# Kernel optimization log

Measured on AMD Instinct MI355X. Metric: run time of the kernel, lower is better.

Reference implementation:

```python
import jax, jax.numpy as jnp
import numpy as np

N, E, D, H, OUT, L, G = 50000, 800000, 128, 128, 128, 5, 512
EMB = L * H  # 640
BN_EPS = 1e-5


def setup_inputs() -> dict:
    key = jax.random.key(0)
    ks = jax.random.split(key, 24)
    s_h = 1.0 / np.sqrt(H)
    s_e = 1.0 / np.sqrt(EMB)
    inp = {
        'x': jax.random.normal(ks[0], (N, D), jnp.float32),
        'edge_index': jax.random.randint(ks[1], (2, E), 0, N, jnp.int32),
        'batch': jnp.sort(jax.random.randint(ks[2], (N,), 0, G, jnp.int32)),
        # per-layer GINConv MLP: Linear(D/H->H), BN(H), ReLU, Linear(H->H). D==H so stackable.
        'conv_W1': jax.random.normal(ks[3], (L, H, H), jnp.float32) * s_h,
        'conv_b1': jnp.zeros((L, H), jnp.float32),
        'conv_g1': jnp.ones((L, H), jnp.float32),
        'conv_be1': jnp.zeros((L, H), jnp.float32),
        'conv_W2': jax.random.normal(ks[4], (L, H, H), jnp.float32) * s_h,
        'conv_b2': jnp.zeros((L, H), jnp.float32),
        'eps': jnp.zeros((L,), jnp.float32),  # train_eps=True, init 0.0
        # outer BatchNorm per layer
        'bn_g': jnp.ones((L, H), jnp.float32),
        'bn_b': jnp.zeros((L, H), jnp.float32),
        # per-layer prediction heads Linear(H -> OUT)
        'pred_W': jax.random.normal(ks[5], (L, H, OUT), jnp.float32) * s_h,
        'pred_b': jnp.zeros((L, OUT), jnp.float32),
        # global_d FF(EMB): 3 stacked Linear(EMB,EMB) + shortcut
        'gW': jax.random.normal(ks[6], (3, EMB, EMB), jnp.float32) * s_e,
        'gb': jnp.zeros((3, EMB), jnp.float32),
        'gsW': jax.random.normal(ks[7], (EMB, EMB), jnp.float32) * s_e,
        'gsb': jnp.zeros((EMB,), jnp.float32),
        # local_d FF(EMB)
        'lW': jax.random.normal(ks[8], (3, EMB, EMB), jnp.float32) * s_e,
        'lb': jnp.zeros((3, EMB), jnp.float32),
        'lsW': jax.random.normal(ks[9], (EMB, EMB), jnp.float32) * s_e,
        'lsb': jnp.zeros((EMB,), jnp.float32),
    }
    return inp


def _bn(h, g, b):
    # BatchNorm1d, training mode: batch stats over node dim (biased var)
    m = jnp.mean(h, axis=0)
    v = jnp.var(h, axis=0)
    return g * (h - m) * jax.lax.rsqrt(v + BN_EPS) + b


def _ff(x, W, b, Ws, bs):
    h = x
    for i in range(3):
        h = jax.nn.relu(h @ W[i] + b[i])
    return h + x @ Ws + bs


def reference(x, edge_index, batch, conv_W1, conv_b1, conv_g1, conv_be1,
              conv_W2, conv_b2, eps, bn_g, bn_b, pred_W, pred_b,
              gW, gb, gsW, gsb, lW, lb, lsW, lsb):
    src, dst = edge_index[0], edge_index[1]
    h = x
    xs = []
    for i in range(L):
        # GINConv: (1+eps)*x_i + sum_{j->i} x_j, then MLP
        agg = jax.ops.segment_sum(h[src], dst, num_segments=N)
        h = (1.0 + eps[i]) * h + agg
        h = _bn(h @ conv_W1[i] + conv_b1[i], conv_g1[i], conv_be1[i])
        h = jax.nn.relu(h)
        h = h @ conv_W2[i] + conv_b2[i]
        h = jax.nn.relu(_bn(h, bn_g[i], bn_b[i]))
        xs.append(h)
    # per-layer graph sum-pool + prediction head (dropout in eval = identity)
    xpool = [jax.ops.segment_sum(xs[i], batch, num_segments=G) @ pred_W[i] + pred_b[i]
             for i in range(L)]
    xcat = jnp.concatenate(xpool, axis=1)            # [G, L*OUT]
    graph_embedding = _ff(xcat, gW, gb, gsW, gsb)     # [G, EMB]
    node_embedding = _ff(jnp.concatenate(xs, axis=1), lW, lb, lsW, lsb)  # [N, EMB]
    return (graph_embedding, node_embedding, xcat)
```

## Files before the change

kernel.cpp:

```cpp
#include <hip/hip_runtime.h>

constexpr int H    = 128;
constexpr int LNUM = 5;
constexpr int NG   = 512;
constexpr int EMB  = 640;
constexpr float BN_EPS = 1e-5f;

typedef __attribute__((ext_vector_type(8))) short bf16x8;
typedef __attribute__((ext_vector_type(4))) float f32x4;

__device__ inline unsigned short f2bf(float f){
  unsigned u = __builtin_bit_cast(unsigned, f);
  u += 0x7FFF + ((u >> 16) & 1);
  return (unsigned short)(u >> 16);
}
__device__ inline float bf2f(unsigned short h){
  unsigned u = ((unsigned)h) << 16;
  return __builtin_bit_cast(float, u);
}

__device__ inline int xcd_swz(int bid, int nwg){
  int q = nwg >> 3, r = nwg & 7;
  int xcd = bid & 7, idx = bid >> 3;
  return (xcd < r ? xcd*(q+1) : r*(q+1) + (xcd-r)*q) + idx;
}

__global__ void k_zerof(float* p, int n){
  int i = blockIdx.x*256 + threadIdx.x;
  if (i < n) p[i] = 0.f;
}
__global__ void k_zeroi(int* p, int n){
  int i = blockIdx.x*256 + threadIdx.x;
  if (i < n) p[i] = 0;
}

__global__ void k_hist(const int* __restrict__ dst, int E, int* deg){
  int e = blockIdx.x*256 + threadIdx.x;
  if (e < E) atomicAdd(&deg[dst[e]], 1);
}

__global__ __launch_bounds__(1024) void k_scan(int* degcur, int* __restrict__ rowptr, int n){
  __shared__ int wsum[16];
  __shared__ int carry;
  int tid = threadIdx.x, wid = tid >> 6, lane = tid & 63;
  if (tid == 0){ carry = 0; rowptr[0] = 0; }
  __syncthreads();
  for (int base = 0; base < n; base += 1024){
    int v = (base + tid < n) ? degcur[base + tid] : 0;
    int s = v;
#pragma unroll
    for (int off = 1; off < 64; off <<= 1){
      int t = __shfl_up(s, off);
      if (lane >= off) s += t;
    }
    if (lane == 63) wsum[wid] = s;
    __syncthreads();
    if (wid == 0 && lane < 16){
      int wv = wsum[lane];
#pragma unroll
      for (int off = 1; off < 16; off <<= 1){
        int t = __shfl_up(wv, off);
        if (lane >= off) wv += t;
      }
      wsum[lane] = wv;
    }
    __syncthreads();
    int incl = s + (wid ? wsum[wid-1] : 0) + carry;
    if (base + tid < n){ rowptr[base + tid + 1] = incl; degcur[base + tid] = incl - v; }
    __syncthreads();
    if (tid == 0) carry += wsum[15];
    __syncthreads();
  }
}

__global__ void k_scatter(const int* __restrict__ src, const int* __restrict__ dst,
                          int E, int* cursor, int* __restrict__ colsrc){
  int e = blockIdx.x*256 + threadIdx.x;
  if (e < E){
    int d = dst[e];
    int pos = atomicAdd(&cursor[d], 1);
    colsrc[pos] = src[e];
  }
}

__global__ void k_gstart(const int* __restrict__ batch, int N, int* __restrict__ gstart){
  int g = blockIdx.x*256 + threadIdx.x;
  if (g <= NG){
    int lo = 0, hi = N;
    while (lo < hi){
      int mid = (lo + hi) >> 1;
      if (batch[mid] < g) lo = mid + 1; else hi = mid;
    }
    gstart[g] = lo;
  }
}

__global__ void k_castT(const float* __restrict__ W, unsigned short* __restrict__ Wt,
                        int K, int Nn, int ldt, int koff){
  __shared__ float sh[32][33];
  const size_t in_off  = (size_t)blockIdx.z * K * Nn;
  const size_t out_off = (size_t)blockIdx.z * Nn * ldt;
  int n0 = blockIdx.x*32, k0 = blockIdx.y*32;
  int tx = threadIdx.x, ty = threadIdx.y;
  for (int r = ty; r < 32; r += 8)
    sh[r][tx] = W[in_off + (size_t)(k0 + r)*Nn + n0 + tx];
  __syncthreads();
  for (int r = ty; r < 32; r += 8)
    Wt[out_off + (size_t)(n0 + r)*ldt + koff + k0 + tx] = f2bf(sh[tx][r]);
}

__global__ void k_bias2(const float* __restrict__ a, const float* __restrict__ b,
                        float* __restrict__ o){
  int i = threadIdx.x;
  o[i] = a[i] + b[i];
}

template<bool IN_BF16>
__global__ __launch_bounds__(256) void k_agg(const void* __restrict__ hin_, int ldh,
                                             const int* __restrict__ rowptr,
                                             const int* __restrict__ colsrc,
                                             const float* __restrict__ epsp,
                                             unsigned short* __restrict__ outp, int nN){
  int node = blockIdx.x*4 + (threadIdx.x >> 6);
  if (node >= nN) return;
  int lane = threadIdx.x & 63;
  float a0, a1;
  if (IN_BF16){
    unsigned u = ((const unsigned*)hin_)[((size_t)node*ldh >> 1) + lane];
    a0 = bf2f((unsigned short)u); a1 = bf2f((unsigned short)(u >> 16));
  } else {
    float2 f = ((const float2*)hin_)[((size_t)node*ldh >> 1) + lane];
    a0 = f.x; a1 = f.y;
  }
  float ep = 1.0f + *epsp;
  a0 *= ep; a1 *= ep;
  int e = rowptr[node], e1 = rowptr[node+1];
  const int ld2 = ldh >> 1;
  for (; e + 4 <= e1; e += 4){
    int s0 = colsrc[e], s1 = colsrc[e+1], s2 = colsrc[e+2], s3 = colsrc[e+3];
    if (IN_BF16){
      unsigned u0 = ((const unsigned*)hin_)[(size_t)s0*ld2 + lane];
      unsigned u1 = ((const unsigned*)hin_)[(size_t)s1*ld2 + lane];
      unsigned u2 = ((const unsigned*)hin_)[(size_t)s2*ld2 + lane];
      unsigned u3 = ((const unsigned*)hin_)[(size_t)s3*ld2 + lane];
      a0 += bf2f((unsigned short)u0) + bf2f((unsigned short)u1)
          + bf2f((unsigned short)u2) + bf2f((unsigned short)u3);
      a1 += bf2f((unsigned short)(u0 >> 16)) + bf2f((unsigned short)(u1 >> 16))
          + bf2f((unsigned short)(u2 >> 16)) + bf2f((unsigned short)(u3 >> 16));
    } else {
      float2 f0 = ((const float2*)hin_)[(size_t)s0*ld2 + lane];
      float2 f1 = ((const float2*)hin_)[(size_t)s1*ld2 + lane];
      float2 f2 = ((const float2*)hin_)[(size_t)s2*ld2 + lane];
      float2 f3 = ((const float2*)hin_)[(size_t)s3*ld2 + lane];
      a0 += f0.x + f1.x + f2.x + f3.x;
      a1 += f0.y + f1.y + f2.y + f3.y;
    }
  }
  for (; e < e1; ++e){
    int s = colsrc[e];
    if (IN_BF16){
      unsigned u = ((const unsigned*)hin_)[(size_t)s*ld2 + lane];
      a0 += bf2f((unsigned short)u); a1 += bf2f((unsigned short)(u >> 16));
    } else {
      float2 f = ((const float2*)hin_)[(size_t)s*ld2 + lane];
      a0 += f.x; a1 += f.y;
    }
  }
  ((unsigned*)outp)[((size_t)node*H >> 1) + lane] =
      (unsigned)f2bf(a0) | ((unsigned)f2bf(a1) << 16);
}

__global__ void k_bnfin(float* sums, float* sumsq,
                        const float* __restrict__ g, const float* __restrict__ b,
                        float* __restrict__ scale, float* __restrict__ shift, float invn){
  int c = threadIdx.x;
  float m = sums[c]*invn;
  float v = sumsq[c]*invn - m*m;
  float inv = rsqrtf(v + BN_EPS);
  float sc = g[c]*inv;
  scale[c] = sc;
  shift[c] = b[c] - m*sc;
  sums[c] = 0.f; sumsq[c] = 0.f;
}

__global__ __launch_bounds__(256) void k_bnapply(const unsigned short* __restrict__ U,
                                                 const float* __restrict__ scale,
                                                 const float* __restrict__ shift,
                                                 unsigned short* __restrict__ out,
                                                 int ldo, int n){
  int i = blockIdx.x*256 + threadIdx.x;
  int total = n * (H/4);
  if (i < total){
    int r = i >> 5;
    int c4 = (i & 31) << 2;
    uint2 up = *(const uint2*)(U + (size_t)r*H + c4);
    float4 sc = *(const float4*)(scale + c4);
    float4 sf = *(const float4*)(shift + c4);
    float a = fmaxf(fmaf(sc.x, bf2f((unsigned short)up.x),        sf.x), 0.f);
    float b = fmaxf(fmaf(sc.y, bf2f((unsigned short)(up.x>>16)),  sf.y), 0.f);
    float c = fmaxf(fmaf(sc.z, bf2f((unsigned short)up.y),        sf.z), 0.f);
    float d = fmaxf(fmaf(sc.w, bf2f((unsigned short)(up.y>>16)),  sf.w), 0.f);
    uint2 o;
    o.x = (unsigned)f2bf(a) | ((unsigned)f2bf(b) << 16);
    o.y = (unsigned)f2bf(c) | ((unsigned)f2bf(d) << 16);
    *(uint2*)(out + (size_t)r*ldo + c4) = o;
  }
}

__global__ __launch_bounds__(320) void k_pool(const unsigned short* __restrict__ xall,
                                              const int* __restrict__ gstart,
                                              float* __restrict__ pooled){
  int g = blockIdx.x;
  int t = threadIdx.x;
  int n0 = gstart[g], n1 = gstart[g+1];
  float a0 = 0.f, a1 = 0.f;
  for (int n = n0; n < n1; ++n){
    unsigned u = ((const unsigned*)xall)[(size_t)n*(EMB/2) + t];
    a0 += bf2f((unsigned short)u); a1 += bf2f((unsigned short)(u >> 16));
  }
  *(float2*)(pooled + (size_t)g*EMB + 2*t) = make_float2(a0, a1);
}

__global__ __launch_bounds__(128) void k_pred(const float* __restrict__ pooled,
                                              const float* __restrict__ W,
                                              const float* __restrict__ b,
                                              float* __restrict__ xcat){
  int g = blockIdx.x, l = blockIdx.y, o = threadIdx.x;
  __shared__ float sh[128];
  sh[o] = pooled[(size_t)g*EMB + l*H + o];
  __syncthreads();
  const float* Wl = W + (size_t)l*H*H;
  float acc = b[l*H + o];
  for (int k = 0; k < H; ++k) acc = fmaf(sh[k], Wl[k*H + o], acc);
  xcat[(size_t)g*EMB + l*H + o] = acc;
}

template<bool RELU, bool OUT_BF16, bool DUAL>
__global__ __launch_bounds__(512) void k_mm(
    const unsigned short* __restrict__ A, int lda,
    const unsigned short* __restrict__ A2,
    const unsigned short* __restrict__ Bt, int ldb,
    const float* __restrict__ bias,
    void* __restrict__ Cv, int ldc,
    int M, int K)
{
  __shared__ union LdsU {
    unsigned short stage[2][2][128*64];
    unsigned short sc16[128*136];
    float          sc32[128*132];
  } u;
  const int tid  = threadIdx.x;
  const int lane = tid & 63;
  const int w    = tid >> 6;
  const int wr   = w >> 2, wc = w & 3;

  const int nwg = gridDim.x * gridDim.y;
  const int bid = blockIdx.y * gridDim.x + blockIdx.x;
  const int wg  = xcd_swz(bid, nwg);
  const int col0 = (wg % gridDim.x) * 128;
  const int row0 = (wg / gridDim.x) * 128;
  const int KA   = DUAL ? (K >> 1) : K;

  const unsigned short *sA[2], *sA2[2], *sB[2];
  int dOff[2];
#pragma unroll
  for (int j = 0; j < 2; ++j){
    int d = w*2048 + j*1024 + lane*16;
    int m = d >> 7;
    int inner = (d & 127) ^ ((m & 7) << 4);
    int gm = row0 + m; if (gm > M-1) gm = M-1;
    sA[j]  = A  + (size_t)gm*lda + (inner >> 1);
    if (DUAL) sA2[j] = A2 + (size_t)gm*lda + (inner >> 1);
    sB[j]  = Bt + (size_t)(col0 + m)*ldb + (inner >> 1);
    dOff[j] = w*2048 + j*1024;
  }

  f32x4 acc[4][2];
#pragma unroll
  for (int i = 0; i < 4; ++i)
#pragma unroll
    for (int j = 0; j < 2; ++j)
      acc[i][j] = (f32x4){0.f, 0.f, 0.f, 0.f};

  auto STAGE = [&](int buf, int kt){
    int k0 = kt*64;
    int ka = k0;
    bool second = DUAL && (k0 >= KA);
    if (second) ka = k0 - KA;
#pragma unroll
    for (int j = 0; j < 2; ++j){
      const unsigned short* srcA = second ? (sA2[j] + ka) : (sA[j] + ka);
      __builtin_amdgcn_global_load_lds(
          (const __attribute__((address_space(1))) void*)srcA,
          (__attribute__((address_space(3))) void*)((char*)&u.stage[buf][0][0] + dOff[j]),
          16, 0, 0);
    }
#pragma unroll
    for (int j = 0; j < 2; ++j)
      __builtin_amdgcn_global_load_lds(
          (const __attribute__((address_space(1))) void*)(sB[j] + k0),
          (__attribute__((address_space(3))) void*)((char*)&u.stage[buf][1][0] + dOff[j]),
          16, 0, 0);
  };

  auto COMPUTE = [&](int buf){
    const char* Ab = (const char*)&u.stage[buf][0][0];
    const char* Bb = (const char*)&u.stage[buf][1][0];
#pragma unroll
    for (int kk = 0; kk < 2; ++kk){
      const int kb = kk*64 + ((lane >> 4) << 4);
      bf16x8 af[4], bfr[2];
#pragma unroll
      for (int i = 0; i < 4; ++i){
        int row = wr*64 + i*16 + (lane & 15);
        int ab  = (row*128 + kb) ^ ((row & 7) << 4);
        af[i] = *(const bf16x8*)(Ab + ab);
      }
#pragma unroll
      for (int j = 0; j < 2; ++j){
        int col = wc*32 + j*16 + (lane & 15);
        int bb  = (col*128 + kb) ^ ((col & 7) << 4);
        bfr[j] = *(const bf16x8*)(Bb + bb);
      }
#pragma unroll
      for (int i = 0; i < 4; ++i)
#pragma unroll
        for (int j = 0; j < 2; ++j)
          acc[i][j] = __builtin_amdgcn_mfma_f32_16x16x32_bf16(af[i], bfr[j], acc[i][j], 0, 0, 0);
    }
  };

  const int NT = K / 64;
  STAGE(0, 0);
  STAGE(1, 1);
  asm volatile("s_waitcnt vmcnt(4)" ::: "memory");
  __syncthreads();

  int cur = 0;
  for (int t = 0; t < NT; ++t){
    COMPUTE(cur);
    if (t == NT-1) break;
    __syncthreads();
    if (t + 2 < NT){
      STAGE(cur, t + 2);
      asm volatile("s_waitcnt vmcnt(4)" ::: "memory");
    } else {
      asm volatile("s_waitcnt vmcnt(0)" ::: "memory");
    }
    __syncthreads();
    cur ^= 1;
  }

  __syncthreads();
  if (OUT_BF16){
#pragma unroll
    for (int j = 0; j < 2; ++j){
      int cl = wc*32 + j*16 + (lane & 15);
      float bs = bias[col0 + cl];
#pragma unroll
      for (int i = 0; i < 4; ++i){
        int rb = wr*64 + i*16 + ((lane >> 4) << 2);
#pragma unroll
        for (int r = 0; r < 4; ++r){
          float v = acc[i][j][r] + bs;
          if (RELU) v = fmaxf(v, 0.f);
          u.sc16[(rb + r)*136 + cl] = f2bf(v);
        }
      }
    }
    __syncthreads();
    unsigned short* Cb = (unsigned short*)Cv;
    for (int idx = tid; idx < 128*16; idx += 512){
      int rr = idx >> 4, seg = idx & 15;
      int grow = row0 + rr;
      if (grow < M){
        uint4 vv = *(const uint4*)&u.sc16[rr*136 + seg*8];
        *(uint4*)(Cb + (size_t)grow*ldc + col0 + seg*8) = vv;
      }
    }
  } else {
#pragma unroll
    for (int j = 0; j < 2; ++j){
      int cl = wc*32 + j*16 + (lane & 15);
      float bs = bias[col0 + cl];
#pragma unroll
      for (int i = 0; i < 4; ++i){
        int rb = wr*64 + i*16 + ((lane >> 4) << 2);
#pragma unroll
        for (int r = 0; r < 4; ++r){
          float v = acc[i][j][r] + bs;
          if (RELU) v = fmaxf(v, 0.f);
          u.sc32[(rb + r)*132 + cl] = v;
        }
      }
    }
    __syncthreads();
    float* Cf = (float*)Cv;
    for (int idx = tid; idx < 128*32; idx += 512){
      int rr = idx >> 5, seg = idx & 31;
      int grow = row0 + rr;
      if (grow < M){
        float4 vv = *(const float4*)&u.sc32[rr*132 + seg*4];
        *(float4*)(Cf + (size_t)grow*ldc + col0 + seg*4) = vv;
      }
    }
  }
}

template<bool PRO_BN, bool STATS>
__global__ __launch_bounds__(512) void k_mmc(
    const unsigned short* __restrict__ A,
    const unsigned short* __restrict__ Bt,
    const float* __restrict__ bias,
    const float* __restrict__ kscale, const float* __restrict__ kshift,
    unsigned short* __restrict__ C, int ldc,
    float* sums, float* sumsq,
    int M)
{
  __shared__ unsigned short shm[2*128*128];
  unsigned short* As = shm;
  unsigned short* Bs = shm + 128*128;
  const int tid  = threadIdx.x;
  const int lane = tid & 63;
  const int w    = tid >> 6;
  const int wr   = w >> 2, wc = w & 3;

  const int wg   = xcd_swz(blockIdx.x, gridDim.x);
  const int row0 = wg * 128;

#pragma unroll
  for (int j = 0; j < 4; ++j){
    int d = w*4096 + j*1024 + lane*16;
    int m = d >> 8;
    int inner = (d & 255) ^ ((m & 15) << 4);
    int gm = row0 + m; if (gm > M-1) gm = M-1;
    __builtin_amdgcn_global_load_lds(
        (const __attribute__((address_space(1))) void*)(A + (size_t)gm*H + (inner >> 1)),
        (__attribute__((address_space(3))) void*)((char*)As + w*4096 + j*1024),
        16, 0, 0);
    __builtin_amdgcn_global_load_lds(
        (const __attribute__((address_space(1))) void*)(Bt + (size_t)m*H + (inner >> 1)),
        (__attribute__((address_space(3))) void*)((char*)Bs + w*4096 + j*1024),
        16, 0, 0);
  }
  asm volatile("s_waitcnt vmcnt(0)" ::: "memory");
  __syncthreads();

  f32x4 acc[4][2];
#pragma unroll
  for (int i = 0; i < 4; ++i)
#pragma unroll
    for (int j = 0; j < 2; ++j)
      acc[i][j] = (f32x4){0.f, 0.f, 0.f, 0.f};

#pragma unroll
  for (int kk = 0; kk < 4; ++kk){
    const int kb = kk*64 + ((lane >> 4) << 4);
    bf16x8 af[4], bfr[2];
#pragma unroll
    for (int i = 0; i < 4; ++i){
      int row = wr*64 + i*16 + (lane & 15);
      int ab  = (row*256 + kb) ^ ((row & 15) << 4);
      af[i] = *(const bf16x8*)((const char*)As + ab);
    }
#pragma unroll
    for (int j = 0; j < 2; ++j){
      int col = wc*32 + j*16 + (lane & 15);
      int bb  = (col*256 + kb) ^ ((col & 15) << 4);
      bfr[j] = *(const bf16x8*)((const char*)Bs + bb);
    }
    if (PRO_BN){
      int k8 = kk*32 + ((lane >> 4) << 3);
      float4 s0 = *(const float4*)(kscale + k8), s1 = *(const float4*)(kscale + k8 + 4);
      float4 f0 = *(const float4*)(kshift + k8), f1 = *(const float4*)(kshift + k8 + 4);
      float sc[8] = {s0.x,s0.y,s0.z,s0.w,s1.x,s1.y,s1.z,s1.w};
      float sf[8] = {f0.x,f0.y,f0.z,f0.w,f1.x,f1.y,f1.z,f1.w};
#pragma unroll
      for (int i = 0; i < 4; ++i){
        bf16x8 a = af[i], o;
#pragma unroll
        for (int jj = 0; jj < 8; ++jj){
          float v = fmaxf(fmaf(sc[jj], bf2f((unsigned short)a[jj]), sf[jj]), 0.f);
          o[jj] = (short)f2bf(v);
        }
        af[i] = o;
      }
    }
#pragma unroll
    for (int i = 0; i < 4; ++i)
#pragma unroll
      for (int j = 0; j < 2; ++j)
        acc[i][j] = __builtin_amdgcn_mfma_f32_16x16x32_bf16(af[i], bfr[j], acc[i][j], 0, 0, 0);
  }

  if (STATS){
#pragma unroll
    for (int j = 0; j < 2; ++j){
      int col = wc*32 + j*16 + (lane & 15);
      float bs = bias[col];
      float s = 0.f, q = 0.f;
#pragma unroll
      for (int i = 0; i < 4; ++i){
        int rb = row0 + wr*64 + i*16 + ((lane >> 4) << 2);
#pragma unroll
        for (int r = 0; r < 4; ++r){
          if (rb + r < M){
            float v = acc[i][j][r] + bs;
            s += v; q += v*v;
          }
        }
      }
      s += __shfl_xor(s, 16); q += __shfl_xor(q, 16);
      s += __shfl_xor(s, 32); q += __shfl_xor(q, 32);
      if (lane < 16){
        atomicAdd(&sums[col], s);
        atomicAdd(&sumsq[col], q);
      }
    }
  }

  __syncthreads();
#pragma unroll
  for (int j = 0; j < 2; ++j){
    int cl = wc*32 + j*16 + (lane & 15);
    float bs = bias[cl];
#pragma unroll
    for (int i = 0; i < 4; ++i){
      int rb = wr*64 + i*16 + ((lane >> 4) << 2);
#pragma unroll
      for (int r = 0; r < 4; ++r)
        shm[(rb + r)*136 + cl] = f2bf(acc[i][j][r] + bs);
    }
  }
  __syncthreads();
  for (int idx = tid; idx < 128*16; idx += 512){
    int rr = idx >> 4, seg = idx & 15;
    int grow = row0 + rr;
    if (grow < M){
      uint4 vv = *(const uint4*)&shm[rr*136 + seg*8];
      *(uint4*)(C + (size_t)grow*ldc + seg*8) = vv;
    }
  }
}

template<bool RELU, bool ADD_D>
__global__ __launch_bounds__(256) void k_gemm64(
    const float* __restrict__ A, int lda,
    const float* __restrict__ B, int ldb,
    const float* __restrict__ bias,
    const float* D, int ldd,
    float* C, int ldc,
    int M, int N, int K)
{
  __shared__ float As[32][68];
  __shared__ float Bs[32][64];
  const int tid  = threadIdx.x;
  const int tx   = tid & 15;
  const int ty   = tid >> 4;
  const int row0 = blockIdx.x * 64;
  const int col0 = blockIdx.y * 64;
  const int am = tid >> 3;
  const int ak = (tid & 7) << 2;
  const int bk = tid >> 4;
  const int bn = (tid & 15) << 2;
  float acc[4][4] = {};

  for (int k0 = 0; k0 < K; k0 += 32){
#pragma unroll
    for (int h = 0; h < 2; ++h){
      int m  = am + h*32;
      int gr = row0 + m;
      float4 v = make_float4(0.f, 0.f, 0.f, 0.f);
      if (gr < M) v = *(const float4*)(A + (size_t)gr*lda + k0 + ak);
      As[ak+0][m]=v.x; As[ak+1][m]=v.y; As[ak+2][m]=v.z; As[ak+3][m]=v.w;
    }
#pragma unroll
    for (int h = 0; h < 2; ++h){
      int kk = bk + h*16;
      *(float4*)(&Bs[kk][bn]) = *(const float4*)(B + (size_t)(k0+kk)*ldb + col0 + bn);
    }
    __syncthreads();
#pragma unroll 8
    for (int k = 0; k < 32; ++k){
      float4 a = *(const float4*)(&As[k][ty<<2]);
      float4 b = *(const float4*)(&Bs[k][tx<<2]);
      float av[4] = {a.x,a.y,a.z,a.w};
      float bv[4] = {b.x,b.y,b.z,b.w};
#pragma unroll
      for (int i = 0; i < 4; ++i)
#pragma unroll
        for (int j = 0; j < 4; ++j)
          acc[i][j] = fmaf(av[i], bv[j], acc[i][j]);
    }
    __syncthreads();
  }

  const int col = col0 + (tx<<2);
  float4 bv = *(const float4*)(bias + col);
#pragma unroll
  for (int i = 0; i < 4; ++i){
    int row = row0 + (ty<<2) + i;
    if (row < M){
      float r[4] = {acc[i][0]+bv.x, acc[i][1]+bv.y, acc[i][2]+bv.z, acc[i][3]+bv.w};
      if (RELU){
#pragma unroll
        for (int j = 0; j < 4; ++j) r[j] = fmaxf(r[j], 0.f);
      }
      if (ADD_D){
        float4 d = *(const float4*)(D + (size_t)row*ldd + col);
        r[0]+=d.x; r[1]+=d.y; r[2]+=d.z; r[3]+=d.w;
      }
      *(float4*)(C + (size_t)row*ldc + col) = make_float4(r[0],r[1],r[2],r[3]);
    }
  }
}

extern "C" void kernel_launch(void* const* d_in, const int* in_sizes, int n_in,
                              void* d_out, int out_size, void* d_ws, size_t ws_size,
                              hipStream_t stream) {
  const float* x        = (const float*)d_in[0];
  const int*   ei       = (const int*)d_in[1];
  const int*   batch    = (const int*)d_in[2];
  const float* conv_W1  = (const float*)d_in[3];
  const float* conv_b1  = (const float*)d_in[4];
  const float* conv_g1  = (const float*)d_in[5];
  const float* conv_be1 = (const float*)d_in[6];
  const float* conv_W2  = (const float*)d_in[7];
  const float* conv_b2  = (const float*)d_in[8];
  const float* epsv     = (const float*)d_in[9];
  const float* bn_g     = (const float*)d_in[10];
  const float* bn_b     = (const float*)d_in[11];
  const float* pred_W   = (const float*)d_in[12];
  const float* pred_b   = (const float*)d_in[13];
  const float* gW       = (const float*)d_in[14];
  const float* gb       = (const float*)d_in[15];
  const float* gsW      = (const float*)d_in[16];
  const float* gsb      = (const float*)d_in[17];
  const float* lW       = (const float*)d_in[18];
  const float* lb       = (const float*)d_in[19];
  const float* lsW      = (const float*)d_in[20];
  const float* lsb      = (const float*)d_in[21];

  const int N = in_sizes[0] / H;
  const int E = in_sizes[1] / 2;
  const int* srcI = ei;
  const int* dstI = ei + E;

  float* out = (float*)d_out;
  float* GE = out;
  float* NE = out + (size_t)NG*EMB;
  float* XC = NE + (size_t)N*EMB;

  unsigned short* xall = (unsigned short*)d_ws;
  unsigned short* h1   = xall + (size_t)N*EMB;
  unsigned short* h2   = h1 + (size_t)N*EMB;
  unsigned short* hpre = h1;
  unsigned short* ub   = h1 + (size_t)N*H;
  unsigned short* tb   = h1 + (size_t)2*N*H;

  float* pooled  = (float*)(h2 + (size_t)N*EMB);
  float* gtmp1   = pooled + (size_t)NG*EMB;
  float* gtmp2   = gtmp1 + (size_t)NG*EMB;
  float* sums    = gtmp2 + (size_t)NG*EMB;
  float* sumsq   = sums + 128;
  float* bnscale = sumsq + 128;
  float* bnshift = bnscale + 128;
  float* biasNE  = bnshift + 128;
  unsigned short* W1t   = (unsigned short*)(biasNE + EMB);
  unsigned short* W2t   = W1t + (size_t)LNUM*H*H;
  unsigned short* lWt01 = W2t + (size_t)LNUM*H*H;
  unsigned short* Wcat  = lWt01 + (size_t)2*EMB*EMB;
  int* rowptr = (int*)(Wcat + (size_t)2*EMB*EMB);
  int* cursor = rowptr + (N + 1);
  int* colsrc = cursor + N;
  int* gstart = colsrc + E;

  k_zerof<<<1, 256, 0, stream>>>(sums, 256);

  k_zeroi<<<(N+255)/256, 256, 0, stream>>>(cursor, N);
  k_hist<<<(E+255)/256, 256, 0, stream>>>(dstI, E, cursor);
  k_scan<<<1, 1024, 0, stream>>>(cursor, rowptr, N);
  k_scatter<<<(E+255)/256, 256, 0, stream>>>(srcI, dstI, E, cursor, colsrc);
  k_gstart<<<(NG+256)/256, 256, 0, stream>>>(batch, N, gstart);

  const dim3 tb32(32, 8);
  k_castT<<<dim3(H/32, H/32, LNUM), tb32, 0, stream>>>(conv_W1, W1t, H, H, H, 0);
  k_castT<<<dim3(H/32, H/32, LNUM), tb32, 0, stream>>>(conv_W2, W2t, H, H, H, 0);
  k_castT<<<dim3(EMB/32, EMB/32, 2), tb32, 0, stream>>>(lW, lWt01, EMB, EMB, EMB, 0);
  k_castT<<<dim3(EMB/32, EMB/32, 1), tb32, 0, stream>>>(lW + (size_t)2*EMB*EMB, Wcat,
                                                        EMB, EMB, 2*EMB, 0);
  k_castT<<<dim3(EMB/32, EMB/32, 1), tb32, 0, stream>>>(lsW, Wcat, EMB, EMB, 2*EMB, EMB);
  k_bias2<<<1, EMB, 0, stream>>>(lb + (size_t)2*EMB, lsb, biasNE);

  const float invn = 1.0f / (float)N;
  const int nrow = (N + 127)/128;

  for (int l = 0; l < LNUM; ++l){
    if (l == 0)
      k_agg<false><<<(N+3)/4, 256, 0, stream>>>(x, H, rowptr, colsrc, epsv, hpre, N);
    else
      k_agg<true><<<(N+3)/4, 256, 0, stream>>>(xall + (size_t)(l-1)*H, EMB, rowptr, colsrc,
                                               epsv + l, hpre, N);

    k_mmc<false,true><<<nrow, 512, 0, stream>>>(
        hpre, W1t + (size_t)l*H*H, conv_b1 + l*H, nullptr, nullptr,
        ub, H, sums, sumsq, N);
    k_bnfin<<<1, 128, 0, stream>>>(sums, sumsq, conv_g1 + l*H, conv_be1 + l*H,
                                   bnscale, bnshift, invn);
    k_mmc<true,true><<<nrow, 512, 0, stream>>>(
        ub, W2t + (size_t)l*H*H, conv_b2 + l*H, bnscale, bnshift,
        tb, H, sums, sumsq, N);
    k_bnfin<<<1, 128, 0, stream>>>(sums, sumsq, bn_g + l*H, bn_b + l*H,
                                   bnscale, bnshift, invn);
    k_bnapply<<<(N*32 + 255)/256, 256, 0, stream>>>(tb, bnscale, bnshift,
                                                    xall + (size_t)l*H, EMB, N);
  }

  k_pool<<<NG, 320, 0, stream>>>(xall, gstart, pooled);
  k_pred<<<dim3(NG, LNUM), 128, 0, stream>>>(pooled, pred_W, pred_b, XC);

  const dim3 gg((NG + 63)/64, EMB/64);
  k_gemm64<false,false><<<gg, 256, 0, stream>>>(XC, EMB, gsW, EMB, gsb,
                                                nullptr, 0, GE, EMB, NG, EMB, EMB);
  k_gemm64<true,false><<<gg, 256, 0, stream>>>(XC, EMB, gW, EMB, gb,
                                               nullptr, 0, gtmp1, EMB, NG, EMB, EMB);
  k_gemm64<true,false><<<gg, 256, 0, stream>>>(gtmp1, EMB, gW + (size_t)EMB*EMB, EMB, gb + EMB,
                                               nullptr, 0, gtmp2, EMB, NG, EMB, EMB);
  k_gemm64<true,true><<<gg, 256, 0, stream>>>(gtmp2, EMB, gW + (size_t)2*EMB*EMB, EMB, gb + 2*EMB,
                                              GE, EMB, GE, EMB, NG, EMB, EMB);

  const dim3 gn(EMB/128, nrow);
  k_mm<true,true,false><<<gn, 512, 0, stream>>>(
      xall, EMB, nullptr, lWt01, EMB, lb, h1, EMB, N, EMB);
  k_mm<true,true,false><<<gn, 512, 0, stream>>>(
      h1, EMB, nullptr, lWt01 + (size_t)EMB*EMB, EMB, lb + EMB, h2, EMB, N, EMB);
  k_mm<false,false,true><<<gn, 512, 0, stream>>>(
      h2, EMB, xall, Wcat, 2*EMB, biasNE, NE, EMB, N, 2*EMB);
}
```

Before: 1.181 ms.

## Fuse neighbor aggregation into first GIN matmul and fold BN finalize into consumers

Neighbor aggregation now runs inside the first per-layer matmul kernel. Each thread gathers 32 features of one node, sums over its neighbors, and writes the bf16 result straight into the LDS A tile, so the hpre buffer is never written to or read back from global memory. BN finalize kernels are removed: the scale and shift are computed from per-layer stat slots inside the second matmul and inside bnapply. Separately, the large node-FF GEMM switches to 32-wide K tiles with a 4-deep LDS ring and a different swizzle. The fused gather uses one thread per 32 columns with a serial neighbor loop, which may expose gather latency and lower occupancy compared with the old wavefront-per-node kernel.

```diff
diff --git a/kernel.cpp b/kernel.cpp
--- a/kernel.cpp
+++ b/kernel.cpp
@@ -113,98 +113,6 @@
                         float* __restrict__ o){
   int i = threadIdx.x;
   o[i] = a[i] + b[i];
-}
-
-template<bool IN_BF16>
-__global__ __launch_bounds__(256) void k_agg(const void* __restrict__ hin_, int ldh,
-                                             const int* __restrict__ rowptr,
-                                             const int* __restrict__ colsrc,
-                                             const float* __restrict__ epsp,
-                                             unsigned short* __restrict__ outp, int nN){
-  int node = blockIdx.x*4 + (threadIdx.x >> 6);
-  if (node >= nN) return;
-  int lane = threadIdx.x & 63;
-  float a0, a1;
-  if (IN_BF16){
-    unsigned u = ((const unsigned*)hin_)[((size_t)node*ldh >> 1) + lane];
-    a0 = bf2f((unsigned short)u); a1 = bf2f((unsigned short)(u >> 16));
-  } else {
-    float2 f = ((const float2*)hin_)[((size_t)node*ldh >> 1) + lane];
-    a0 = f.x; a1 = f.y;
-  }
-  float ep = 1.0f + *epsp;
-  a0 *= ep; a1 *= ep;
-  int e = rowptr[node], e1 = rowptr[node+1];
-  const int ld2 = ldh >> 1;
-  for (; e + 4 <= e1; e += 4){
-    int s0 = colsrc[e], s1 = colsrc[e+1], s2 = colsrc[e+2], s3 = colsrc[e+3];
-    if (IN_BF16){
-      unsigned u0 = ((const unsigned*)hin_)[(size_t)s0*ld2 + lane];
-      unsigned u1 = ((const unsigned*)hin_)[(size_t)s1*ld2 + lane];
-      unsigned u2 = ((const unsigned*)hin_)[(size_t)s2*ld2 + lane];
-      unsigned u3 = ((const unsigned*)hin_)[(size_t)s3*ld2 + lane];
-      a0 += bf2f((unsigned short)u0) + bf2f((unsigned short)u1)
-          + bf2f((unsigned short)u2) + bf2f((unsigned short)u3);
-      a1 += bf2f((unsigned short)(u0 >> 16)) + bf2f((unsigned short)(u1 >> 16))
-          + bf2f((unsigned short)(u2 >> 16)) + bf2f((unsigned short)(u3 >> 16));
-    } else {
-      float2 f0 = ((const float2*)hin_)[(size_t)s0*ld2 + lane];
-      float2 f1 = ((const float2*)hin_)[(size_t)s1*ld2 + lane];
-      float2 f2 = ((const float2*)hin_)[(size_t)s2*ld2 + lane];
-      float2 f3 = ((const float2*)hin_)[(size_t)s3*ld2 + lane];
-      a0 += f0.x + f1.x + f2.x + f3.x;
-      a1 += f0.y + f1.y + f2.y + f3.y;
-    }
-  }
-  for (; e < e1; ++e){
-    int s = colsrc[e];
-    if (IN_BF16){
-      unsigned u = ((const unsigned*)hin_)[(size_t)s*ld2 + lane];
-      a0 += bf2f((unsigned short)u); a1 += bf2f((unsigned short)(u >> 16));
-    } else {
-      float2 f = ((const float2*)hin_)[(size_t)s*ld2 + lane];
-      a0 += f.x; a1 += f.y;
-    }
-  }
-  ((unsigned*)outp)[((size_t)node*H >> 1) + lane] =
-      (unsigned)f2bf(a0) | ((unsigned)f2bf(a1) << 16);
-}
-
-__global__ void k_bnfin(float* sums, float* sumsq,
-                        const float* __restrict__ g, const float* __restrict__ b,
-                        float* __restrict__ scale, float* __restrict__ shift, float invn){
-  int c = threadIdx.x;
-  float m = sums[c]*invn;
-  float v = sumsq[c]*invn - m*m;
-  float inv = rsqrtf(v + BN_EPS);
-  float sc = g[c]*inv;
-  scale[c] = sc;
-  shift[c] = b[c] - m*sc;
-  sums[c] = 0.f; sumsq[c] = 0.f;
-}
-
-__global__ __launch_bounds__(256) void k_bnapply(const unsigned short* __restrict__ U,
-                                                 const float* __restrict__ scale,
-                                                 const float* __restrict__ shift,
-                                                 unsigned short* __restrict__ out,
-                                                 int ldo, int n){
-  int i = blockIdx.x*256 + threadIdx.x;
-  int total = n * (H/4);
-  if (i < total){
-    int r = i >> 5;
-    int c4 = (i & 31) << 2;
-    uint2 up = *(const uint2*)(U + (size_t)r*H + c4);
-    float4 sc = *(const float4*)(scale + c4);
-    float4 sf = *(const float4*)(shift + c4);
-    float a = fmaxf(fmaf(sc.x, bf2f((unsigned short)up.x),        sf.x), 0.f);
-    float b = fmaxf(fmaf(sc.y, bf2f((unsigned short)(up.x>>16)),  sf.y), 0.f);
-    float c = fmaxf(fmaf(sc.z, bf2f((unsigned short)up.y),        sf.z), 0.f);
-    float d = fmaxf(fmaf(sc.w, bf2f((unsigned short)(up.y>>16)),  sf.w), 0.f);
-    uint2 o;
-    o.x = (unsigned)f2bf(a) | ((unsigned)f2bf(b) << 16);
-    o.y = (unsigned)f2bf(c) | ((unsigned)f2bf(d) << 16);
-    *(uint2*)(out + (size_t)r*ldo + c4) = o;
-  }
 }
 
 __global__ __launch_bounds__(320) void k_pool(const unsigned short* __restrict__ xall,
@@ -245,7 +153,7 @@
     int M, int K)
 {
   __shared__ union LdsU {
-    unsigned short stage[2][2][128*64];
+    unsigned short stage[4][8192];
     unsigned short sc16[128*136];
     float          sc32[128*132];
   } u;
@@ -261,19 +169,23 @@
   const int row0 = (wg / gridDim.x) * 128;
   const int KA   = DUAL ? (K >> 1) : K;
 
-  const unsigned short *sA[2], *sA2[2], *sB[2];
-  int dOff[2];
-#pragma unroll
-  for (int j = 0; j < 2; ++j){
-    int d = w*2048 + j*1024 + lane*16;
-    int m = d >> 7;
-    int inner = (d & 127) ^ ((m & 7) << 4);
+  const unsigned short *sA, *sA2p = nullptr, *sB;
+  {
+    int d = w*1024 + lane*16;
+    int m = d >> 6;
+    int inner = (d & 63) ^ ((((m >> 1) & 3)) << 4);
     int gm = row0 + m; if (gm > M-1) gm = M-1;
-    sA[j]  = A  + (size_t)gm*lda + (inner >> 1);
-    if (DUAL) sA2[j] = A2 + (size_t)gm*lda + (inner >> 1);
-    sB[j]  = Bt + (size_t)(col0 + m)*ldb + (inner >> 1);
-    dOff[j] = w*2048 + j*1024;
-  }
+    sA = A + (size_t)gm*lda + (inner >> 1);
+    if (DUAL) sA2p = A2 + (size_t)gm*lda + (inner >> 1);
+  }
+  {
+    int d = w*1024 + lane*16;
+    int m = d >> 6;
+    int inner = (d & 63) ^ ((((m >> 1) & 3)) << 4);
+    sB = Bt + (size_t)(col0 + m)*ldb + (inner >> 1);
+  }
+  const int dAoff = w*1024;
+  const int dBoff = 8192 + w*1024;
 
   f32x4 acc[4][2];
 #pragma unroll
@@ -283,72 +195,55 @@
       acc[i][j] = (f32x4){0.f, 0.f, 0.f, 0.f};
 
   auto STAGE = [&](int buf, int kt){
-    int k0 = kt*64;
-    int ka = k0;
+    int k0 = kt*32, ka = k0;
     bool second = DUAL && (k0 >= KA);
     if (second) ka = k0 - KA;
+    char* base = (char*)&u.stage[buf][0];
+    const unsigned short* s = second ? (sA2p + ka) : (sA + ka);
+    __builtin_amdgcn_global_load_lds(
+        (const __attribute__((address_space(1))) void*)s,
+        (__attribute__((address_space(3))) void*)(base + dAoff), 16, 0, 0);
+    __builtin_amdgcn_global_load_lds(
+        (const __attribute__((address_space(1))) void*)(sB + k0),
+        (__attribute__((address_space(3))) void*)(base + dBoff), 16, 0, 0);
+  };
+
+  auto COMPUTE = [&](int buf){
+    const char* Ab = (const char*)&u.stage[buf][0];
+    const char* Bb = Ab + 8192;
+    const int kb = (lane >> 4) << 4;
+    bf16x8 af[4], bfr[2];
+#pragma unroll
+    for (int i = 0; i < 4; ++i){
+      int row = wr*64 + i*16 + (lane & 15);
+      af[i] = *(const bf16x8*)(Ab + ((row*64 + kb) ^ ((((row >> 1) & 3)) << 4)));
+    }
 #pragma unroll
     for (int j = 0; j < 2; ++j){
-      const unsigned short* srcA = second ? (sA2[j] + ka) : (sA[j] + ka);
-      __builtin_amdgcn_global_load_lds(
-          (const __attribute__((address_space(1))) void*)srcA,
-          (__attribute__((address_space(3))) void*)((char*)&u.stage[buf][0][0] + dOff[j]),
-          16, 0, 0);
-    }
-#pragma unroll
-    for (int j = 0; j < 2; ++j)
-      __builtin_amdgcn_global_load_lds(
-          (const __attribute__((address_space(1))) void*)(sB[j] + k0),
-          (__attribute__((address_space(3))) void*)((char*)&u.stage[buf][1][0] + dOff[j]),
-          16, 0, 0);
+      int col = wc*32 + j*16 + (lane & 15);
+      bfr[j] = *(const bf16x8*)(Bb + ((col*64 + kb) ^ ((((col >> 1) & 3)) << 4)));
+    }
+#pragma unroll
+    for (int i = 0; i < 4; ++i)
+#pragma unroll
+      for (int j = 0; j < 2; ++j)
+        acc[i][j] = __builtin_amdgcn_mfma_f32_16x16x32_bf16(af[i], bfr[j], acc[i][j], 0, 0, 0);
   };
 
-  auto COMPUTE = [&](int buf){
-    const char* Ab = (const char*)&u.stage[buf][0][0];
-    const char* Bb = (const char*)&u.stage[buf][1][0];
-#pragma unroll
-    for (int kk = 0; kk < 2; ++kk){
-      const int kb = kk*64 + ((lane >> 4) << 4);
-      bf16x8 af[4], bfr[2];
-#pragma unroll
-      for (int i = 0; i < 4; ++i){
-        int row = wr*64 + i*16 + (lane & 15);
-        int ab  = (row*128 + kb) ^ ((row & 7) << 4);
-        af[i] = *(const bf16x8*)(Ab + ab);
-      }
-#pragma unroll
-      for (int j = 0; j < 2; ++j){
-        int col = wc*32 + j*16 + (lane & 15);
-        int bb  = (col*128 + kb) ^ ((col & 7) << 4);
-        bfr[j] = *(const bf16x8*)(Bb + bb);
-      }
-#pragma unroll
-      for (int i = 0; i < 4; ++i)
-#pragma unroll
-        for (int j = 0; j < 2; ++j)
-          acc[i][j] = __builtin_amdgcn_mfma_f32_16x16x32_bf16(af[i], bfr[j], acc[i][j], 0, 0, 0);
-    }
-  };
-
-  const int NT = K / 64;
+  const int NT = K / 32;
   STAGE(0, 0);
   STAGE(1, 1);
-  asm volatile("s_waitcnt vmcnt(4)" ::: "memory");
-  __syncthreads();
-
-  int cur = 0;
   for (int t = 0; t < NT; ++t){
-    COMPUTE(cur);
-    if (t == NT-1) break;
-    __syncthreads();
     if (t + 2 < NT){
-      STAGE(cur, t + 2);
+      STAGE((t + 2) & 3, t + 2);
       asm volatile("s_waitcnt vmcnt(4)" ::: "memory");
+    } else if (t + 1 < NT){
+      asm volatile("s_waitcnt vmcnt(2)" ::: "memory");
     } else {
       asm volatile("s_waitcnt vmcnt(0)" ::: "memory");
     }
     __syncthreads();
-    cur ^= 1;
+    COMPUTE(t & 3);
   }
 
   __syncthreads();
@@ -407,19 +302,197 @@
   }
 }
 
-template<bool PRO_BN, bool STATS>
-__global__ __launch_bounds__(512) void k_mmc(
-    const unsigned short* __restrict__ A,
+template<bool IN_BF16>
+__global__ __launch_bounds__(512) void k_mmca(
+    const void* __restrict__ hin, int ldh,
+    const int* __restrict__ rowptr, const int* __restrict__ colsrc,
+    const float* __restrict__ epsp,
     const unsigned short* __restrict__ Bt,
     const float* __restrict__ bias,
-    const float* __restrict__ kscale, const float* __restrict__ kshift,
     unsigned short* __restrict__ C, int ldc,
-    float* sums, float* sumsq,
+    float* __restrict__ sums, float* __restrict__ sumsq,
     int M)
 {
   __shared__ unsigned short shm[2*128*128];
   unsigned short* As = shm;
-  unsigned short* Bs = shm + 128*128;
+  unsigned short* Bs = shm + 16384;
+  const int tid  = threadIdx.x;
+  const int lane = tid & 63;
+  const int w    = tid >> 6;
+  const int wr   = w >> 2, wc = w & 3;
+
+  const int wg   = xcd_swz(blockIdx.x, gridDim.x);
+  const int row0 = wg * 128;
+
+#pragma unroll
+  for (int j = 0; j < 4; ++j){
+    int d = w*4096 + j*1024 + lane*16;
+    int m = d >> 8;
+    int inner = (d & 255) ^ ((m & 15) << 4);
+    __builtin_amdgcn_global_load_lds(
+        (const __attribute__((address_space(1))) void*)(Bt + (size_t)m*H + (inner >> 1)),
+        (__attribute__((address_space(3))) void*)((char*)Bs + w*4096 + j*1024),
+        16, 0, 0);
+  }
+
+  {
+    int r  = tid >> 2;
+    int c0 = (tid & 3) << 5;
+    int node = row0 + r; if (node > M-1) node = M-1;
+    float ep = 1.0f + *epsp;
+    float a[32];
+    if (IN_BF16){
+      const unsigned short* src = (const unsigned short*)hin + (size_t)node*ldh + c0;
+#pragma unroll
+      for (int q = 0; q < 4; ++q){
+        uint2 v = *(const uint2*)(src + q*8);
+        a[q*8+0] = ep*bf2f((unsigned short)v.x);  a[q*8+1] = ep*bf2f((unsigned short)(v.x>>16));
+        uint2 v2 = *(const uint2*)(src + q*8 + 4);
+        a[q*8+2] = ep*bf2f((unsigned short)v.y);  a[q*8+3] = ep*bf2f((unsigned short)(v.y>>16));
+        a[q*8+4] = ep*bf2f((unsigned short)v2.x); a[q*8+5] = ep*bf2f((unsigned short)(v2.x>>16));
+        a[q*8+6] = ep*bf2f((unsigned short)v2.y); a[q*8+7] = ep*bf2f((unsigned short)(v2.y>>16));
+      }
+    } else {
+      const float* src = (const float*)hin + (size_t)node*ldh + c0;
+#pragma unroll
+      for (int q = 0; q < 32; q += 4){
+        float4 f = *(const float4*)(src + q);
+        a[q] = ep*f.x; a[q+1] = ep*f.y; a[q+2] = ep*f.z; a[q+3] = ep*f.w;
+      }
+    }
+    int e = rowptr[node], e1 = rowptr[node+1];
+    for (; e < e1; ++e){
+      int s = colsrc[e];
+      if (IN_BF16){
+        const unsigned short* p = (const unsigned short*)hin + (size_t)s*ldh + c0;
+        uint4 v0 = *(const uint4*)(p);
+        uint4 v1 = *(const uint4*)(p + 8);
+        uint4 v2 = *(const uint4*)(p + 16);
+        uint4 v3 = *(const uint4*)(p + 24);
+        const unsigned* uu[4] = {(const unsigned*)&v0, (const unsigned*)&v1,
+                                 (const unsigned*)&v2, (const unsigned*)&v3};
+#pragma unroll
+        for (int q = 0; q < 4; ++q)
+#pragma unroll
+          for (int k = 0; k < 4; ++k){
+            unsigned x = uu[q][k];
+            a[q*8 + 2*k]     += bf2f((unsigned short)x);
+            a[q*8 + 2*k + 1] += bf2f((unsigned short)(x >> 16));
+          }
+      } else {
+        const float* p = (const float*)hin + (size_t)s*ldh + c0;
+#pragma unroll
+        for (int q = 0; q < 32; q += 4){
+          float4 f = *(const float4*)(p + q);
+          a[q] += f.x; a[q+1] += f.y; a[q+2] += f.z; a[q+3] += f.w;
+        }
+      }
+    }
+#pragma unroll
+    for (int q = 0; q < 4; ++q){
+      unsigned pk[4];
+#pragma unroll
+      for (int k = 0; k < 4; ++k)
+        pk[k] = (unsigned)f2bf(a[q*8 + 2*k]) | ((unsigned)f2bf(a[q*8 + 2*k + 1]) << 16);
+      int byte = (r*256 + (tid & 3)*64 + q*16) ^ ((r & 15) << 4);
+      *(uint4*)((char*)As + byte) = *(uint4*)pk;
+    }
+  }
+
+  asm volatile("s_waitcnt vmcnt(0)" ::: "memory");
+  __syncthreads();
+
+  f32x4 acc[4][2];
+#pragma unroll
+  for (int i = 0; i < 4; ++i)
+#pragma unroll
+    for (int j = 0; j < 2; ++j)
+      acc[i][j] = (f32x4){0.f, 0.f, 0.f, 0.f};
+
+#pragma unroll
+  for (int kk = 0; kk < 4; ++kk){
+    const int kb = kk*64 + ((lane >> 4) << 4);
+    bf16x8 af[4], bfr[2];
+#pragma unroll
+    for (int i = 0; i < 4; ++i){
+      int row = wr*64 + i*16 + (lane & 15);
+      af[i] = *(const bf16x8*)((const char*)As + ((row*256 + kb) ^ ((row & 15) << 4)));
+    }
+#pragma unroll
+    for (int j = 0; j < 2; ++j){
+      int col = wc*32 + j*16 + (lane & 15);
+      bfr[j] = *(const bf16x8*)((const char*)Bs + ((col*256 + kb) ^ ((col & 15) << 4)));
+    }
+#pragma unroll
+    for (int i = 0; i < 4; ++i)
+#pragma unroll
+      for (int j = 0; j < 2; ++j)
+        acc[i][j] = __builtin_amdgcn_mfma_f32_16x16x32_bf16(af[i], bfr[j], acc[i][j], 0, 0, 0);
+  }
+
+#pragma unroll
+  for (int j = 0; j < 2; ++j){
+    int col = wc*32 + j*16 + (lane & 15);
+    float bs = bias[col];
+    float s = 0.f, q = 0.f;
+#pragma unroll
+    for (int i = 0; i < 4; ++i){
+      int rb = row0 + wr*64 + i*16 + ((lane >> 4) << 2);
+#pragma unroll
+      for (int r = 0; r < 4; ++r){
+        if (rb + r < M){
+          float v = acc[i][j][r] + bs;
+          s += v; q += v*v;
+        }
+      }
+    }
+    s += __shfl_xor(s, 16); q += __shfl_xor(q, 16);
+    s += __shfl_xor(s, 32); q += __shfl_xor(q, 32);
+    if (lane < 16){
+      atomicAdd(&sums[col], s);
+      atomicAdd(&sumsq[col], q);
+    }
+  }
+
+  __syncthreads();
+#pragma unroll
+  for (int j = 0; j < 2; ++j){
+    int cl = wc*32 + j*16 + (lane & 15);
+    float bs = bias[cl];
+#pragma unroll
+    for (int i = 0; i < 4; ++i){
+      int rb = wr*64 + i*16 + ((lane >> 4) << 2);
+#pragma unroll
+      for (int r = 0; r < 4; ++r)
+        shm[(rb + r)*136 + cl] = f2bf(acc[i][j][r] + bs);
+    }
+  }
+  __syncthreads();
+  for (int idx = tid; idx < 128*16; idx += 512){
+    int rr = idx >> 4, seg = idx & 15;
+    int grow = row0 + rr;
+    if (grow < M){
+      uint4 vv = *(const uint4*)&shm[rr*136 + seg*8];
+      *(uint4*)(C + (size_t)grow*ldc + seg*8) = vv;
+    }
+  }
+}
+
+__global__ __launch_bounds__(512) void k_mmc2(
+    const unsigned short* __restrict__ A,
+    const unsigned short* __restrict__ Bt,
+    const float* __restrict__ bias,
+    const float* __restrict__ statin,
+    const float* __restrict__ g1, const float* __restrict__ be1,
+    float invn,
+    unsigned short* __restrict__ C, int ldc,
+    float* __restrict__ sums, float* __restrict__ sumsq,
+    int M)
+{
+  __shared__ unsigned short shm[2*128*128];
+  __shared__ float bnsc[128], bnsf[128];
+  unsigned short* As = shm;
+  unsigned short* Bs = shm + 16384;
   const int tid  = threadIdx.x;
   const int lane = tid & 63;
   const int w    = tid >> 6;
@@ -443,6 +516,16 @@
         (__attribute__((address_space(3))) void*)((char*)Bs + w*4096 + j*1024),
         16, 0, 0);
   }
+
+  if (tid < 128){
+    float m = statin[tid]*invn;
+    float v = statin[128 + tid]*invn - m*m;
+    float inv = rsqrtf(v + BN_EPS);
+    float sc = g1[tid]*inv;
+    bnsc[tid] = sc;
+    bnsf[tid] = be1[tid] - m*sc;
+  }
+
   asm volatile("s_waitcnt vmcnt(0)" ::: "memory");
   __syncthreads();
 
@@ -460,27 +543,25 @@
 #pragma unroll
     for (int i = 0; i < 4; ++i){
       int row = wr*64 + i*16 + (lane & 15);
-      int ab  = (row*256 + kb) ^ ((row & 15) << 4);
-      af[i] = *(const bf16x8*)((const char*)As + ab);
+      af[i] = *(const bf16x8*)((const char*)As + ((row*256 + kb) ^ ((row & 15) << 4)));
     }
 #pragma unroll
     for (int j = 0; j < 2; ++j){
       int col = wc*32 + j*16 + (lane & 15);
-      int bb  = (col*256 + kb) ^ ((col & 15) << 4);
-      bfr[j] = *(const bf16x8*)((const char*)Bs + bb);
-    }
-    if (PRO_BN){
+      bfr[j] = *(const bf16x8*)((const char*)Bs + ((col*256 + kb) ^ ((col & 15) << 4)));
+    }
+    {
       int k8 = kk*32 + ((lane >> 4) << 3);
-      float4 s0 = *(const float4*)(kscale + k8), s1 = *(const float4*)(kscale + k8 + 4);
-      float4 f0 = *(const float4*)(kshift + k8), f1 = *(const float4*)(kshift + k8 + 4);
+      float4 s0 = *(const float4*)(&bnsc[k8]), s1 = *(const float4*)(&bnsc[k8 + 4]);
+      float4 f0 = *(const float4*)(&bnsf[k8]), f1 = *(const float4*)(&bnsf[k8 + 4]);
       float sc[8] = {s0.x,s0.y,s0.z,s0.w,s1.x,s1.y,s1.z,s1.w};
       float sf[8] = {f0.x,f0.y,f0.z,f0.w,f1.x,f1.y,f1.z,f1.w};
 #pragma unroll
       for (int i = 0; i < 4; ++i){
-        bf16x8 a = af[i], o;
+        bf16x8 aa = af[i], o;
 #pragma unroll
         for (int jj = 0; jj < 8; ++jj){
-          float v = fmaxf(fmaf(sc[jj], bf2f((unsigned short)a[jj]), sf[jj]), 0.f);
+          float v = fmaxf(fmaf(sc[jj], bf2f((unsigned short)aa[jj]), sf[jj]), 0.f);
           o[jj] = (short)f2bf(v);
         }
         af[i] = o;
@@ -493,29 +574,27 @@
         acc[i][j] = __builtin_amdgcn_mfma_f32_16x16x32_bf16(af[i], bfr[j], acc[i][j], 0, 0, 0);
   }
 
-  if (STATS){
-#pragma unroll
-    for (int j = 0; j < 2; ++j){
-      int col = wc*32 + j*16 + (lane & 15);
-      float bs = bias[col];
-      float s = 0.f, q = 0.f;
-#pragma unroll
-      for (int i = 0; i < 4; ++i){
-        int rb = row0 + wr*64 + i*16 + ((lane >> 4) << 2);
-#pragma unroll
-        for (int r = 0; r < 4; ++r){
-          if (rb + r < M){
-            float v = acc[i][j][r] + bs;
-            s += v; q += v*v;
-          }
+#pragma unroll
+  for (int j = 0; j < 2; ++j){
+    int col = wc*32 + j*16 + (lane & 15);
+    float bs = bias[col];
+    float s = 0.f, q = 0.f;
+#pragma unroll
+    for (int i = 0; i < 4; ++i){
+      int rb = row0 + wr*64 + i*16 + ((lane >> 4) << 2);
+#pragma unroll
+      for (int r = 0; r < 4; ++r){
+        if (rb + r < M){
+          float v = acc[i][j][r] + bs;
+          s += v; q += v*v;
         }
       }
-      s += __shfl_xor(s, 16); q += __shfl_xor(q, 16);
-      s += __shfl_xor(s, 32); q += __shfl_xor(q, 32);
-      if (lane < 16){
-        atomicAdd(&sums[col], s);
-        atomicAdd(&sumsq[col], q);
-      }
+    }
+    s += __shfl_xor(s, 16); q += __shfl_xor(q, 16);
+    s += __shfl_xor(s, 32); q += __shfl_xor(q, 32);
+    if (lane < 16){
+      atomicAdd(&sums[col], s);
+      atomicAdd(&sumsq[col], q);
     }
   }
 
@@ -540,6 +619,40 @@
       uint4 vv = *(const uint4*)&shm[rr*136 + seg*8];
       *(uint4*)(C + (size_t)grow*ldc + seg*8) = vv;
     }
+  }
+}
+
+__global__ __launch_bounds__(256) void k_bnapply(const unsigned short* __restrict__ U,
+                                                 const float* __restrict__ statp,
+                                                 const float* __restrict__ g,
+                                                 const float* __restrict__ b,
+                                                 float invn,
+                                                 unsigned short* __restrict__ out,
+                                                 int ldo, int n){
+  int i = blockIdx.x*256 + threadIdx.x;
+  int total = n * (H/4);
+  if (i < total){
+    int r = i >> 5;
+    int c4 = (i & 31) << 2;
+    float4 sm = *(const float4*)(statp + c4);
+    float4 sq = *(const float4*)(statp + 128 + c4);
+    float4 gg = *(const float4*)(g + c4);
+    float4 bb = *(const float4*)(b + c4);
+    float m0 = sm.x*invn, m1 = sm.y*invn, m2 = sm.z*invn, m3 = sm.w*invn;
+    float s0 = gg.x*rsqrtf(sq.x*invn - m0*m0 + BN_EPS);
+    float s1 = gg.y*rsqrtf(sq.y*invn - m1*m1 + BN_EPS);
+    float s2 = gg.z*rsqrtf(sq.z*invn - m2*m2 + BN_EPS);
+    float s3 = gg.w*rsqrtf(sq.w*invn - m3*m3 + BN_EPS);
+    float f0 = bb.x - m0*s0, f1 = bb.y - m1*s1, f2 = bb.z - m2*s2, f3 = bb.w - m3*s3;
+    uint2 up = *(const uint2*)(U + (size_t)r*H + c4);
+    float a = fmaxf(fmaf(s0, bf2f((unsigned short)up.x),       f0), 0.f);
+    float c = fmaxf(fmaf(s1, bf2f((unsigned short)(up.x>>16)), f1), 0.f);
+    float d = fmaxf(fmaf(s2, bf2f((unsigned short)up.y),       f2), 0.f);
+    float e = fmaxf(fmaf(s3, bf2f((unsigned short)(up.y>>16)), f3), 0.f);
+    uint2 o;
+    o.x = (unsigned)f2bf(a) | ((unsigned)f2bf(c) << 16);
+    o.y = (unsigned)f2bf(d) | ((unsigned)f2bf(e) << 16);
+    *(uint2*)(out + (size_t)r*ldo + c4) = o;
   }
 }
 
@@ -654,18 +767,14 @@
   unsigned short* xall = (unsigned short*)d_ws;
   unsigned short* h1   = xall + (size_t)N*EMB;
   unsigned short* h2   = h1 + (size_t)N*EMB;
-  unsigned short* hpre = h1;
-  unsigned short* ub   = h1 + (size_t)N*H;
-  unsigned short* tb   = h1 + (size_t)2*N*H;
+  unsigned short* ub   = h1;
+  unsigned short* tb   = h1 + (size_t)N*H;
 
   float* pooled  = (float*)(h2 + (size_t)N*EMB);
   float* gtmp1   = pooled + (size_t)NG*EMB;
   float* gtmp2   = gtmp1 + (size_t)NG*EMB;
-  float* sums    = gtmp2 + (size_t)NG*EMB;
-  float* sumsq   = sums + 128;
-  float* bnscale = sumsq + 128;
-  float* bnshift = bnscale + 128;
-  float* biasNE  = bnshift + 128;
+  float* slots   = gtmp2 + (size_t)NG*EMB;
+  float* biasNE  = slots + 2560;
   unsigned short* W1t   = (unsigned short*)(biasNE + EMB);
   unsigned short* W2t   = W1t + (size_t)LNUM*H*H;
   unsigned short* lWt01 = W2t + (size_t)LNUM*H*H;
@@ -675,7 +784,7 @@
   int* colsrc = cursor + N;
   int* gstart = colsrc + E;
 
-  k_zerof<<<1, 256, 0, stream>>>(sums, 256);
+  k_zerof<<<10, 256, 0, stream>>>(slots, 2560);
 
   k_zeroi<<<(N+255)/256, 256, 0, stream>>>(cursor, N);
   k_hist<<<(E+255)/256, 256, 0, stream>>>(dstI, E, cursor);
@@ -696,24 +805,27 @@
   const int nrow = (N + 127)/128;
 
   for (int l = 0; l < LNUM; ++l){
+    float* slot1 = slots + (size_t)l*512;
+    float* slot2 = slot1 + 256;
+
     if (l == 0)
-      k_agg<false><<<(N+3)/4, 256, 0, stream>>>(x, H, rowptr, colsrc, epsv, hpre, N);
+      k_mmca<false><<<nrow, 512, 0, stream>>>(
+          x, H, rowptr, colsrc, epsv, W1t, conv_b1,
+          ub, H, slot1, slot1 + 128, N);
     else
-      k_agg<true><<<(N+3)/4, 256, 0, stream>>>(xall + (size_t)(l-1)*H, EMB, rowptr, colsrc,
-                                               epsv + l, hpre, N);
-
-    k_mmc<false,true><<<nrow, 512, 0, stream>>>(
-        hpre, W1t + (size_t)l*H*H, conv_b1 + l*H, nullptr, nullptr,
-        ub, H, sums, sumsq, N);
-    k_bnfin<<<1, 128, 0, stream>>>(sums, sumsq, conv_g1 + l*H, conv_be1 + l*H,
-                                   bnscale, bnshift, invn);
-    k_mmc<true,true><<<nrow, 512, 0, stream>>>(
-        ub, W2t + (size_t)l*H*H, conv_b2 + l*H, bnscale, bnshift,
-        tb, H, sums, sumsq, N);
-    k_bnfin<<<1, 128, 0, stream>>>(sums, sumsq, bn_g + l*H, bn_b + l*H,
-                                   bnscale, bnshift, invn);
-    k_bnapply<<<(N*32 + 255)/256, 256, 0, stream>>>(tb, bnscale, bnshift,
-                                                    xall + (size_t)l*H, EMB, N);
+      k_mmca<true><<<nrow, 512, 0, stream>>>(
+          xall + (size_t)(l-1)*H, EMB, rowptr, colsrc, epsv + l,
+          W1t + (size_t)l*H*H, conv_b1 + l*H,
+          ub, H, slot1, slot1 + 128, N);
+
+    k_mmc2<<<nrow, 512, 0, stream>>>(
+        ub, W2t + (size_t)l*H*H, conv_b2 + l*H,
+        slot1, conv_g1 + l*H, conv_be1 + l*H, invn,
+        tb, H, slot2, slot2 + 128, N);
+
+    k_bnapply<<<(N*32 + 255)/256, 256, 0, stream>>>(
+        tb, slot2, bn_g + l*H, bn_b + l*H, invn,
+        xall + (size_t)l*H, EMB, N);
   }
 
   k_pool<<<NG, 320, 0, stream>>>(xall, gstart, pooled);
```

After: 1.148 ms. 1.03x faster.
